# Performance work log

Measured on AMD Instinct MI355X. Metric: run time of the kernel, lower is better.

## Reference

```python
import jax, jax.numpy as jnp
import numpy as np

QP = 127.0          # signed symmetric 8-bit: Qp = 2**(8-1)-1
MIN_RANGE = 1e-6


def _ste_round(q):
    # round_pass: straight-through estimator round
    return q + jax.lax.stop_gradient(jnp.round(q) - q)


def _quant_per_token(x):
    # symmetric per-token: amax over last dim, keepdim
    s = jnp.clip(jnp.max(jnp.abs(x), axis=-1, keepdims=True), MIN_RANGE, None) / QP
    return _ste_round(x / s), s


def _quant_per_tensor(w):
    s = jnp.clip(jnp.max(jnp.abs(w)), MIN_RANGE, None) / QP
    return _ste_round(w / s), s


def _qlinear(x2d, w, b):
    # fake-quant linear: quantize act per-token, weight per-tensor,
    # int-domain matmul, bias added before dequant rescale (faithful to source)
    qx, sx = _quant_per_token(x2d)      # [N,K], [N,1]
    qw, sw = _quant_per_tensor(w)       # [M,K], scalar
    out = jnp.matmul(qx, qw.T) + b[None, :]
    return out * (sx * sw)              # [N,M]


def setup_inputs() -> dict:
    key = jax.random.key(0)
    k1, k2, k3, k4, k5 = jax.random.split(key, 5)
    B, S, D, H = 64, 197, 768, 3072
    return {
        "x": jax.random.normal(k1, (B, S, D), dtype=jnp.float32),
        "w1": jax.random.normal(k2, (H, D), dtype=jnp.float32) * 0.02,
        "b1": jax.random.normal(k3, (H,), dtype=jnp.float32) * 0.02,
        "w2": jax.random.normal(k4, (D, H), dtype=jnp.float32) * 0.02,
        "b2": jax.random.normal(k5, (D,), dtype=jnp.float32) * 0.02,
    }


def reference(x, w1, b1, w2, b2):
    B, S, D = x.shape
    x2d = x.reshape(-1, D)                         # view(-1, x.size(-1))
    h = _qlinear(x2d, w1, b1)                      # fc1
    h = jax.nn.gelu(h, approximate=False)          # ViT Mlp activation (exact GELU)
    o = _qlinear(h, w2, b2)                        # fc2
    return o.reshape(B, S, -1)
```

## Files before the change

kernel.cpp:

```cpp
#include <hip/hip_runtime.h>
#include <stdint.h>

#define QPF  127.0f
#define MINR 1e-6f

typedef int v4i __attribute__((ext_vector_type(4)));
typedef float f4v __attribute__((ext_vector_type(4)));
typedef _Float16 h4v __attribute__((ext_vector_type(4)));
typedef _Float16 h8 __attribute__((ext_vector_type(8)));
typedef signed char c8 __attribute__((ext_vector_type(8)));

__device__ __forceinline__ float wave_max64(float v) {
  v = fmaxf(v, __shfl_xor(v, 32, 64));
  v = fmaxf(v, __shfl_xor(v, 16, 64));
  v = fmaxf(v, __shfl_xor(v, 8, 64));
  v = fmaxf(v, __shfl_xor(v, 4, 64));
  v = fmaxf(v, __shfl_xor(v, 2, 64));
  v = fmaxf(v, __shfl_xor(v, 1, 64));
  return v;
}

__device__ __forceinline__ float gelu_exact(float x) {
  float z = fabsf(x) * 0.70710678118654752440f;
  float t = __builtin_amdgcn_rcpf(fmaf(0.3275911f, z, 1.0f));
  float p = fmaf(fmaf(fmaf(fmaf(1.061405429f, t, -1.453152027f), t,
                           1.421413741f), t, -0.284496736f), t, 0.254829592f) * t;
  float e = __expf(-z * z);
  float erfz = fmaf(-p, e, 1.0f);
  float cdf = fmaf(0.5f, copysignf(erfz, x), 0.5f);
  return x * cdf;
}

__device__ __forceinline__ void gl2lds16(const void* g, void* l) {
  __builtin_amdgcn_global_load_lds(
      (const __attribute__((address_space(1))) int*)g,
      (__attribute__((address_space(3))) int*)l,
      16, 0, 0);
}

__device__ __forceinline__ int xcd_swizzle(int flat, int nwg) {
  const int xcd = flat & 7;
  const int idx = flat >> 3;
  const int q = nwg >> 3, r = nwg & 7;
  const int base = (xcd < r) ? xcd * (q + 1) : r * (q + 1) + (xcd - r) * q;
  return base + idx;
}

__global__ __launch_bounds__(256) void pre_kernel(
    const float* __restrict__ w1, const float* __restrict__ w2, int n4,
    const float* __restrict__ x, signed char* __restrict__ qx,
    float* __restrict__ sx, unsigned* __restrict__ amaxh,
    float* __restrict__ partial, int K, int nTok) {
  __shared__ float red[4];
  const int b = blockIdx.x;
  const int tid = threadIdx.x;
  const int lane = tid & 63, wvi = tid >> 6;

  if (b < 1024) {
    const float4* w4 = (const float4*)(b < 512 ? w1 : w2);
    const int bb = b & 511;
    float m = 0.f;
    for (int i = bb * 256 + tid; i < n4; i += 512 * 256) {
      float4 v = w4[i];
      m = fmaxf(m, fmaxf(fmaxf(fabsf(v.x), fabsf(v.y)),
                         fmaxf(fabsf(v.z), fabsf(v.w))));
    }
    m = wave_max64(m);
    if (lane == 0) red[wvi] = m;
    __syncthreads();
    if (tid == 0)
      partial[b] = fmaxf(fmaxf(red[0], red[1]), fmaxf(red[2], red[3]));
  } else {
    const int token = (b - 1024) * 4 + wvi;
    if (token < nTok) {
      const int k4 = K >> 2;
      const float4* xr = (const float4*)(x + (size_t)token * K);
      float m = 0.f;
      for (int i = lane; i < k4; i += 64) {
        float4 v = xr[i];
        m = fmaxf(m, fmaxf(fmaxf(fabsf(v.x), fabsf(v.y)),
                           fmaxf(fabsf(v.z), fabsf(v.w))));
      }
      m = wave_max64(m);
      const float s = fmaxf(m, MINR) / QPF;
      const float rs = 1.0f / s;
      if (lane == 0) { sx[token] = s; amaxh[token] = 0u; }
      char4* q4 = (char4*)(qx + (size_t)token * K);
      for (int i = lane; i < k4; i += 64) {
        float4 v = xr[i];
        char4 c;
        c.x = (signed char)(int)rintf(v.x * rs);
        c.y = (signed char)(int)rintf(v.y * rs);
        c.z = (signed char)(int)rintf(v.z * rs);
        c.w = (signed char)(int)rintf(v.w * rs);
        q4[i] = c;
      }
    }
  }
}

__global__ __launch_bounds__(256) void wquant2_kernel(
    const float* __restrict__ w1, const float* __restrict__ w2, int n4,
    const float* __restrict__ partial, unsigned* __restrict__ wamax,
    signed char* __restrict__ q1, signed char* __restrict__ q2) {
  __shared__ float red[4];
  const int tid = threadIdx.x;
  const int lane = tid & 63, wvi = tid >> 6;
  const int y = blockIdx.y;
  float m = fmaxf(partial[y * 512 + tid], partial[y * 512 + 256 + tid]);
  m = wave_max64(m);
  if (lane == 0) red[wvi] = m;
  __syncthreads();
  const float M = fmaxf(fmaxf(red[0], red[1]), fmaxf(red[2], red[3]));
  if (blockIdx.x == 0 && tid == 0) wamax[y] = __float_as_uint(M);
  const float s = fmaxf(M, MINR) / QPF;
  const float rs = 1.0f / s;
  const float4* w4 = (const float4*)(y ? w2 : w1);
  char4* q4 = (char4*)(y ? q2 : q1);
  for (int i = blockIdx.x * 256 + tid; i < n4; i += gridDim.x * 256) {
    float4 v = w4[i];
    char4 c;
    c.x = (signed char)(int)rintf(v.x * rs);
    c.y = (signed char)(int)rintf(v.y * rs);
    c.z = (signed char)(int)rintf(v.z * rs);
    c.w = (signed char)(int)rintf(v.w * rs);
    q4[i] = c;
  }
}

__global__ __launch_bounds__(256) void hquant4_kernel(
    const _Float16* __restrict__ h, const unsigned* __restrict__ amaxbits,
    signed char* __restrict__ qh, float* __restrict__ sh, int K) {
  const int token = blockIdx.x * 4 + (threadIdx.x >> 6);
  const int lane = threadIdx.x & 63;
  const float s = fmaxf(__uint_as_float(amaxbits[token]), MINR) / QPF;
  const float rs = 1.0f / s;
  if (lane == 0) sh[token] = s;
  const h8* hr = (const h8*)(h + (size_t)token * K);
  c8* qr = (c8*)(qh + (size_t)token * K);
  for (int i = lane; i < (K >> 3); i += 64) {
    h8 v = hr[i];
    c8 c;
#pragma unroll
    for (int j = 0; j < 8; j++)
      c[j] = (signed char)(int)rintf((float)v[j] * rs);
    qr[i] = c;
  }
}

__global__ __launch_bounds__(256, 2) void gemm1_i8(
    const signed char* __restrict__ A, const signed char* __restrict__ B,
    const float* __restrict__ bias, const float* __restrict__ sA,
    const unsigned* __restrict__ sBbits, _Float16* __restrict__ out,
    unsigned* __restrict__ amax_out, int N, int K, int Mout) {
  __shared__ __align__(16) signed char lds[3 * 24576];

  const int t = threadIdx.x;
  const int lane = t & 63;
  const int wv = t >> 6;
  const int wm = wv >> 1;
  const int wn = wv & 1;

  const int nwg = gridDim.x * gridDim.y;
  const int wg = xcd_swizzle(blockIdx.x + gridDim.x * blockIdx.y, nwg);
  const int colBlk = (wg % gridDim.x) * 256;
  const int rowBlk = (wg / gridDim.x) * 128;

  const int kb = (((lane & 3) ^ ((lane >> 3) & 3)) * 16);
  const int rr = lane >> 2;

  const signed char* gp[6];
  int ldo[6];
#pragma unroll
  for (int j = 0; j < 6; j++) {
    const int c = wv + 4 * j;
    if (c < 8) {
      int r = rowBlk + c * 16 + rr;
      if (r > N - 1) r = N - 1;
      gp[j] = A + (size_t)r * K + kb;
      ldo[j] = c * 1024;
    } else {
      const int r = colBlk + (c - 8) * 16 + rr;
      gp[j] = B + (size_t)r * K + kb;
      ldo[j] = 8192 + (c - 8) * 1024;
    }
  }

  const v4i vzero = {0, 0, 0, 0};
  v4i acc[4][8];
#pragma unroll
  for (int i = 0; i < 4; i++)
#pragma unroll
    for (int j = 0; j < 8; j++) acc[i][j] = vzero;

  const int swz = ((lane >> 4) ^ ((lane >> 1) & 3)) * 16;
  const int aoff = (wm * 64 + (lane & 15)) * 64 + swz;
  const int boff = 8192 + (wn * 128 + (lane & 15)) * 64 + swz;

  const int T = K >> 6;

  auto issue = [&](int bufo) {
#pragma unroll
    for (int j = 0; j < 6; j++) {
      gl2lds16(gp[j], lds + bufo + ldo[j]);
      gp[j] += 64;
    }
  };

  issue(0);
  issue(24576);

  int cur = 0;
  for (int kt = 0; kt < T; ++kt) {
    asm volatile("" ::: "memory");
    if (kt < T - 1)
      __builtin_amdgcn_s_waitcnt(0x0076);
    else
      __builtin_amdgcn_s_waitcnt(0x0070);
    __builtin_amdgcn_s_barrier();
    asm volatile("" ::: "memory");

    if (kt + 2 < T) {
      int pf = cur + 49152;
      if (pf >= 73728) pf -= 73728;
      issue(pf);
    }

    v4i a[4], b[8];
#pragma unroll
    for (int mi = 0; mi < 4; mi++)
      a[mi] = *(const v4i*)(lds + cur + aoff + mi * 1024);
#pragma unroll
    for (int ni = 0; ni < 8; ni++)
      b[ni] = *(const v4i*)(lds + cur + boff + ni * 1024);
#pragma unroll
    for (int mi = 0; mi < 4; mi++)
#pragma unroll
      for (int ni = 0; ni < 8; ni++)
        acc[mi][ni] = __builtin_amdgcn_mfma_i32_16x16x64_i8(b[ni], a[mi],
                                                            acc[mi][ni], 0, 0, 0);
    cur += 24576;
    if (cur >= 73728) cur = 0;
  }

  const float sB = fmaxf(__uint_as_float(*sBbits), MINR) / QPF;
  const int col0 = colBlk + wn * 128 + (lane >> 4) * 4;

  f4v bv[8];
#pragma unroll
  for (int ni = 0; ni < 8; ni++) bv[ni] = *(const f4v*)(bias + col0 + ni * 16);

#pragma unroll
  for (int mi = 0; mi < 4; mi++) {
    const int grow = rowBlk + wm * 64 + mi * 16 + (lane & 15);
    const float ss = ((grow < N) ? sA[grow] : 0.f) * sB;
    float rmax = 0.f;
#pragma unroll
    for (int ni = 0; ni < 8; ni++) {
      h4v hv;
#pragma unroll
      for (int r = 0; r < 4; r++) {
        float v = ((float)acc[mi][ni][r] + bv[ni][r]) * ss;
        v = gelu_exact(v);
        rmax = fmaxf(rmax, fabsf(v));
        hv[r] = (_Float16)v;
      }
      if (grow < N)
        *(h4v*)(out + (size_t)grow * Mout + col0 + ni * 16) = hv;
    }
    rmax = fmaxf(rmax, __shfl_xor(rmax, 16, 64));
    rmax = fmaxf(rmax, __shfl_xor(rmax, 32, 64));
    if (lane < 16 && grow < N)
      atomicMax(amax_out + grow, __float_as_uint(rmax));
  }
}

__global__ __launch_bounds__(256, 2) void gemm2_i8(
    const signed char* __restrict__ A, const signed char* __restrict__ B,
    const float* __restrict__ bias, const float* __restrict__ sA,
    const unsigned* __restrict__ sBbits, float* __restrict__ out,
    int N, int K, int Mout) {
  __shared__ __align__(16) signed char lds[3 * 24576];

  const int t = threadIdx.x;
  const int lane = t & 63;
  const int wv = t >> 6;
  const int wm = wv >> 1;
  const int wn = wv & 1;

  const int nwg = gridDim.x * gridDim.y;
  const int wg = xcd_swizzle(blockIdx.x + gridDim.x * blockIdx.y, nwg);
  const int colBlk = (wg % gridDim.x) * 128;
  const int rowBlk = (wg / gridDim.x) * 256;

  const int kb = (((lane & 3) ^ ((lane >> 3) & 3)) * 16);
  const int rr = lane >> 2;

  const signed char* gp[6];
  int ldo[6];
#pragma unroll
  for (int j = 0; j < 6; j++) {
    const int c = wv + 4 * j;
    if (c < 16) {
      int r = rowBlk + c * 16 + rr;
      if (r > N - 1) r = N - 1;
      gp[j] = A + (size_t)r * K + kb;
      ldo[j] = c * 1024;
    } else {
      const int r = colBlk + (c - 16) * 16 + rr;
      gp[j] = B + (size_t)r * K + kb;
      ldo[j] = 16384 + (c - 16) * 1024;
    }
  }

  const v4i vzero = {0, 0, 0, 0};
  v4i acc[8][4];
#pragma unroll
  for (int i = 0; i < 8; i++)
#pragma unroll
    for (int j = 0; j < 4; j++) acc[i][j] = vzero;

  const int swz = ((lane >> 4) ^ ((lane >> 1) & 3)) * 16;
  const int aoff = (wm * 128 + (lane & 15)) * 64 + swz;
  const int boff = 16384 + (wn * 64 + (lane & 15)) * 64 + swz;

  const int T = K >> 6;

  auto issue = [&](int bufo) {
#pragma unroll
    for (int j = 0; j < 6; j++) {
      gl2lds16(gp[j], lds + bufo + ldo[j]);
      gp[j] += 64;
    }
  };

  issue(0);
  issue(24576);

  int cur = 0;
  for (int kt = 0; kt < T; ++kt) {
    asm volatile("" ::: "memory");
    if (kt < T - 1)
      __builtin_amdgcn_s_waitcnt(0x0076);
    else
      __builtin_amdgcn_s_waitcnt(0x0070);
    __builtin_amdgcn_s_barrier();
    asm volatile("" ::: "memory");

    if (kt + 2 < T) {
      int pf = cur + 49152;
      if (pf >= 73728) pf -= 73728;
      issue(pf);
    }

    v4i a[8], b[4];
#pragma unroll
    for (int mi = 0; mi < 8; mi++)
      a[mi] = *(const v4i*)(lds + cur + aoff + mi * 1024);
#pragma unroll
    for (int ni = 0; ni < 4; ni++)
      b[ni] = *(const v4i*)(lds + cur + boff + ni * 1024);
#pragma unroll
    for (int mi = 0; mi < 8; mi++)
#pragma unroll
      for (int ni = 0; ni < 4; ni++)
        acc[mi][ni] = __builtin_amdgcn_mfma_i32_16x16x64_i8(b[ni], a[mi],
                                                            acc[mi][ni], 0, 0, 0);
    cur += 24576;
    if (cur >= 73728) cur = 0;
  }

  const float sB = fmaxf(__uint_as_float(*sBbits), MINR) / QPF;
  const int col0 = colBlk + wn * 64 + (lane >> 4) * 4;

  f4v bv[4];
#pragma unroll
  for (int ni = 0; ni < 4; ni++) bv[ni] = *(const f4v*)(bias + col0 + ni * 16);

#pragma unroll
  for (int mi = 0; mi < 8; mi++) {
    const int grow = rowBlk + wm * 128 + mi * 16 + (lane & 15);
    const float ss = ((grow < N) ? sA[grow] : 0.f) * sB;
#pragma unroll
    for (int ni = 0; ni < 4; ni++) {
      f4v o;
#pragma unroll
      for (int r = 0; r < 4; r++)
        o[r] = ((float)acc[mi][ni][r] + bv[ni][r]) * ss;
      if (grow < N)
        *(f4v*)(out + (size_t)grow * Mout + col0 + ni * 16) = o;
    }
  }
}

extern "C" void kernel_launch(void* const* d_in, const int* in_sizes, int n_in,
                              void* d_out, int out_size, void* d_ws, size_t ws_size,
                              hipStream_t stream) {
  const float* x  = (const float*)d_in[0];
  const float* w1 = (const float*)d_in[1];
  const float* b1 = (const float*)d_in[2];
  const float* w2 = (const float*)d_in[3];
  const float* b2 = (const float*)d_in[4];

  const int H = in_sizes[2];
  const int D = in_sizes[4];
  const int N = in_sizes[0] / D;
  float* out = (float*)d_out;

  char* ws = (char*)d_ws;
  auto alloc = [&](size_t bytes) {
    char* p = ws;
    ws += (bytes + 255) & ~(size_t)255;
    return p;
  };
  signed char* qx  = (signed char*)alloc((size_t)N * D);
  signed char* qw1 = (signed char*)alloc((size_t)H * D);
  signed char* qw2 = (signed char*)alloc((size_t)H * D);
  signed char* qh  = (signed char*)alloc((size_t)N * H);
  float*    sx     = (float*)alloc((size_t)N * 4);
  float*    sh     = (float*)alloc((size_t)N * 4);
  unsigned* amaxh  = (unsigned*)alloc((size_t)N * 4);
  unsigned* wamax  = (unsigned*)alloc(256);
  float*    partial= (float*)alloc(1024 * 4);
  _Float16* h      = (_Float16*)alloc((size_t)N * H * 2);
  (void)ws_size;

  const int n4w = (H * D) >> 2;

  pre_kernel<<<1024 + (N + 3) / 4, 256, 0, stream>>>(w1, w2, n4w, x, qx, sx,
                                                     amaxh, partial, D, N);
  wquant2_kernel<<<dim3(512, 2), 256, 0, stream>>>(w1, w2, n4w, partial, wamax,
                                                   qw1, qw2);

  dim3 g1(H / 256, (N + 127) / 128);
  gemm1_i8<<<g1, 256, 0, stream>>>(qx, qw1, b1, sx, wamax + 0, h, amaxh,
                                   N, D, H);
  hquant4_kernel<<<N / 4, 256, 0, stream>>>(h, amaxh, qh, sh, H);

  dim3 g2(D / 128, (N + 255) / 256);
  gemm2_i8<<<g2, 256, 0, stream>>>(qh, qw2, b2, sh, wamax + 1, out, N, H, D);
}
```

Baseline: 238.6 us.

## Enlarge gemm1 tile to 256x256 with 8 waves and phased MFMA/prefetch interleave

gemm1 now uses a 256x256 output tile with 512 threads (8 waves in a 2x4 layout), so each block reuses both operands over more output and the grid has fewer blocks. The k-step is split into four phases, each loading two A fragments, issuing one async global-to-LDS prefetch and running eight MFMAs at raised priority, with barriers between phases. This interleaves memory and matrix work and cuts LDS reads per MFMA. In exchange LDS use grows to 96 KB per block and there is more barrier synchronisation, which may limit occupancy; with N=12608 there are fewer, larger blocks, which could hurt load balance across CUs.

```diff
diff --git a/kernel.cpp b/kernel.cpp
--- a/kernel.cpp
+++ b/kernel.cpp
@@ -148,115 +148,160 @@
   }
 }
 
-__global__ __launch_bounds__(256, 2) void gemm1_i8(
+#define PHASE_MMA(MI0, MI1)                                                    \
+  acc[MI0][0] = __builtin_amdgcn_mfma_i32_16x16x64_i8(b0, a0, acc[MI0][0], 0, 0, 0); \
+  acc[MI0][1] = __builtin_amdgcn_mfma_i32_16x16x64_i8(b1, a0, acc[MI0][1], 0, 0, 0); \
+  acc[MI0][2] = __builtin_amdgcn_mfma_i32_16x16x64_i8(b2, a0, acc[MI0][2], 0, 0, 0); \
+  acc[MI0][3] = __builtin_amdgcn_mfma_i32_16x16x64_i8(b3, a0, acc[MI0][3], 0, 0, 0); \
+  acc[MI1][0] = __builtin_amdgcn_mfma_i32_16x16x64_i8(b0, a1, acc[MI1][0], 0, 0, 0); \
+  acc[MI1][1] = __builtin_amdgcn_mfma_i32_16x16x64_i8(b1, a1, acc[MI1][1], 0, 0, 0); \
+  acc[MI1][2] = __builtin_amdgcn_mfma_i32_16x16x64_i8(b2, a1, acc[MI1][2], 0, 0, 0); \
+  acc[MI1][3] = __builtin_amdgcn_mfma_i32_16x16x64_i8(b3, a1, acc[MI1][3], 0, 0, 0);
+
+__global__ __launch_bounds__(512, 2) void gemm1_i8(
     const signed char* __restrict__ A, const signed char* __restrict__ B,
     const float* __restrict__ bias, const float* __restrict__ sA,
     const unsigned* __restrict__ sBbits, _Float16* __restrict__ out,
     unsigned* __restrict__ amax_out, int N, int K, int Mout) {
-  __shared__ __align__(16) signed char lds[3 * 24576];
+  __shared__ __align__(16) signed char lds[3 * 32768];
 
   const int t = threadIdx.x;
   const int lane = t & 63;
   const int wv = t >> 6;
-  const int wm = wv >> 1;
-  const int wn = wv & 1;
+  const int wm = wv >> 2;
+  const int wn = wv & 3;
 
   const int nwg = gridDim.x * gridDim.y;
   const int wg = xcd_swizzle(blockIdx.x + gridDim.x * blockIdx.y, nwg);
   const int colBlk = (wg % gridDim.x) * 256;
-  const int rowBlk = (wg / gridDim.x) * 128;
+  const int rowBlk = (wg / gridDim.x) * 256;
 
   const int kb = (((lane & 3) ^ ((lane >> 3) & 3)) * 16);
   const int rr = lane >> 2;
 
-  const signed char* gp[6];
-  int ldo[6];
-#pragma unroll
-  for (int j = 0; j < 6; j++) {
-    const int c = wv + 4 * j;
-    if (c < 8) {
+  const signed char* gp[4];
+  int ldo[4];
+#pragma unroll
+  for (int j = 0; j < 4; j++) {
+    const int c = wv + 8 * j;
+    if (c < 16) {
       int r = rowBlk + c * 16 + rr;
       if (r > N - 1) r = N - 1;
       gp[j] = A + (size_t)r * K + kb;
       ldo[j] = c * 1024;
     } else {
-      const int r = colBlk + (c - 8) * 16 + rr;
+      const int r = colBlk + (c - 16) * 16 + rr;
       gp[j] = B + (size_t)r * K + kb;
-      ldo[j] = 8192 + (c - 8) * 1024;
+      ldo[j] = 16384 + (c - 16) * 1024;
     }
   }
 
   const v4i vzero = {0, 0, 0, 0};
-  v4i acc[4][8];
-#pragma unroll
-  for (int i = 0; i < 4; i++)
-#pragma unroll
-    for (int j = 0; j < 8; j++) acc[i][j] = vzero;
+  v4i acc[8][4];
+#pragma unroll
+  for (int i = 0; i < 8; i++)
+#pragma unroll
+    for (int j = 0; j < 4; j++) acc[i][j] = vzero;
 
   const int swz = ((lane >> 4) ^ ((lane >> 1) & 3)) * 16;
-  const int aoff = (wm * 64 + (lane & 15)) * 64 + swz;
-  const int boff = 8192 + (wn * 128 + (lane & 15)) * 64 + swz;
+  const int aoff = (wm * 128 + (lane & 15)) * 64 + swz;
+  const int boff = 16384 + (wn * 64 + (lane & 15)) * 64 + swz;
 
   const int T = K >> 6;
 
-  auto issue = [&](int bufo) {
-#pragma unroll
-    for (int j = 0; j < 6; j++) {
-      gl2lds16(gp[j], lds + bufo + ldo[j]);
-      gp[j] += 64;
-    }
+  auto issue1 = [&](int bufo, int j) {
+    gl2lds16(gp[j], lds + bufo + ldo[j]);
+    gp[j] += 64;
   };
 
-  issue(0);
-  issue(24576);
+#pragma unroll
+  for (int j = 0; j < 4; j++) issue1(0, j);
+#pragma unroll
+  for (int j = 0; j < 4; j++) issue1(32768, j);
 
   int cur = 0;
   for (int kt = 0; kt < T; ++kt) {
     asm volatile("" ::: "memory");
     if (kt < T - 1)
-      __builtin_amdgcn_s_waitcnt(0x0076);
+      __builtin_amdgcn_s_waitcnt(0x0074);
     else
       __builtin_amdgcn_s_waitcnt(0x0070);
     __builtin_amdgcn_s_barrier();
     asm volatile("" ::: "memory");
 
-    if (kt + 2 < T) {
-      int pf = cur + 49152;
-      if (pf >= 73728) pf -= 73728;
-      issue(pf);
-    }
-
-    v4i a[4], b[8];
-#pragma unroll
-    for (int mi = 0; mi < 4; mi++)
-      a[mi] = *(const v4i*)(lds + cur + aoff + mi * 1024);
-#pragma unroll
-    for (int ni = 0; ni < 8; ni++)
-      b[ni] = *(const v4i*)(lds + cur + boff + ni * 1024);
-#pragma unroll
-    for (int mi = 0; mi < 4; mi++)
-#pragma unroll
-      for (int ni = 0; ni < 8; ni++)
-        acc[mi][ni] = __builtin_amdgcn_mfma_i32_16x16x64_i8(b[ni], a[mi],
-                                                            acc[mi][ni], 0, 0, 0);
-    cur += 24576;
-    if (cur >= 73728) cur = 0;
+    const bool pf = (kt + 2 < T);
+    int pfo = cur + 65536;
+    if (pfo >= 98304) pfo -= 98304;
+
+    v4i a0, a1, b0, b1, b2, b3;
+
+    b0 = *(const v4i*)(lds + cur + boff);
+    b1 = *(const v4i*)(lds + cur + boff + 1024);
+    b2 = *(const v4i*)(lds + cur + boff + 2048);
+    b3 = *(const v4i*)(lds + cur + boff + 3072);
+    a0 = *(const v4i*)(lds + cur + aoff);
+    a1 = *(const v4i*)(lds + cur + aoff + 1024);
+    if (pf) issue1(pfo, 0);
+    asm volatile("" ::: "memory");
+    __builtin_amdgcn_s_waitcnt(0xC07F);
+    __builtin_amdgcn_s_setprio(1);
+    PHASE_MMA(0, 1)
+    __builtin_amdgcn_s_setprio(0);
+    asm volatile("" ::: "memory");
+    __builtin_amdgcn_s_barrier();
+    asm volatile("" ::: "memory");
+
+    a0 = *(const v4i*)(lds + cur + aoff + 2048);
+    a1 = *(const v4i*)(lds + cur + aoff + 3072);
+    if (pf) issue1(pfo, 1);
+    asm volatile("" ::: "memory");
+    __builtin_amdgcn_s_waitcnt(0xC07F);
+    __builtin_amdgcn_s_setprio(1);
+    PHASE_MMA(2, 3)
+    __builtin_amdgcn_s_setprio(0);
+    asm volatile("" ::: "memory");
+    __builtin_amdgcn_s_barrier();
+    asm volatile("" ::: "memory");
+
+    a0 = *(const v4i*)(lds + cur + aoff + 4096);
+    a1 = *(const v4i*)(lds + cur + aoff + 5120);
+    if (pf) issue1(pfo, 2);
+    asm volatile("" ::: "memory");
+    __builtin_amdgcn_s_waitcnt(0xC07F);
+    __builtin_amdgcn_s_setprio(1);
+    PHASE_MMA(4, 5)
+    __builtin_amdgcn_s_setprio(0);
+    asm volatile("" ::: "memory");
+    __builtin_amdgcn_s_barrier();
+    asm volatile("" ::: "memory");
+
+    a0 = *(const v4i*)(lds + cur + aoff + 6144);
+    a1 = *(const v4i*)(lds + cur + aoff + 7168);
+    if (pf) issue1(pfo, 3);
+    asm volatile("" ::: "memory");
+    __builtin_amdgcn_s_waitcnt(0xC07F);
+    __builtin_amdgcn_s_setprio(1);
+    PHASE_MMA(6, 7)
+    __builtin_amdgcn_s_setprio(0);
+
+    cur += 32768;
+    if (cur >= 98304) cur = 0;
   }
 
   const float sB = fmaxf(__uint_as_float(*sBbits), MINR) / QPF;
-  const int col0 = colBlk + wn * 128 + (lane >> 4) * 4;
-
-  f4v bv[8];
-#pragma unroll
-  for (int ni = 0; ni < 8; ni++) bv[ni] = *(const f4v*)(bias + col0 + ni * 16);
-
-#pragma unroll
-  for (int mi = 0; mi < 4; mi++) {
-    const int grow = rowBlk + wm * 64 + mi * 16 + (lane & 15);
+  const int col0 = colBlk + wn * 64 + (lane >> 4) * 4;
+
+  f4v bv[4];
+#pragma unroll
+  for (int ni = 0; ni < 4; ni++) bv[ni] = *(const f4v*)(bias + col0 + ni * 16);
+
+#pragma unroll
+  for (int mi = 0; mi < 8; mi++) {
+    const int grow = rowBlk + wm * 128 + mi * 16 + (lane & 15);
     const float ss = ((grow < N) ? sA[grow] : 0.f) * sB;
     float rmax = 0.f;
 #pragma unroll
-    for (int ni = 0; ni < 8; ni++) {
+    for (int ni = 0; ni < 4; ni++) {
       h4v hv;
 #pragma unroll
       for (int r = 0; r < 4; r++) {
@@ -432,8 +477,8 @@
   wquant2_kernel<<<dim3(512, 2), 256, 0, stream>>>(w1, w2, n4w, partial, wamax,
                                                    qw1, qw2);
 
-  dim3 g1(H / 256, (N + 127) / 128);
-  gemm1_i8<<<g1, 256, 0, stream>>>(qx, qw1, b1, sx, wamax + 0, h, amaxh,
+  dim3 g1(H / 256, (N + 255) / 256);
+  gemm1_i8<<<g1, 512, 0, stream>>>(qx, qw1, b1, sx, wamax + 0, h, amaxh,
                                    N, D, H);
   hquant4_kernel<<<N / 4, 256, 0, stream>>>(h, amaxh, qh, sh, H);
 
```

New measurement: 252.6 us. 5.9% more time.
